# Kernel tuning notes

Measured on AMD Instinct MI355X. Metric: run time of the kernel, lower is better.

Reference implementation:

```python
import jax, jax.numpy as jnp
import numpy as np

D_MODEL = 1024
N_HEAD = 16
HEAD_DIM = D_MODEL // N_HEAD


def setup_inputs() -> dict:
    key = jax.random.key(0)
    ks = jax.random.split(key, 11)
    B, L = 1, 2048
    s = 1.0 / np.sqrt(D_MODEL)
    return {
        "q": jax.random.normal(ks[0], (B, L, D_MODEL), jnp.float32),
        "k": jax.random.normal(ks[1], (B, L, D_MODEL), jnp.float32),
        "v": jax.random.normal(ks[2], (B, L, D_MODEL), jnp.float32),
        "w_q": jax.random.normal(ks[3], (D_MODEL, D_MODEL), jnp.float32) * s,
        "b_q": jax.random.normal(ks[4], (D_MODEL,), jnp.float32) * s,
        "w_k": jax.random.normal(ks[5], (D_MODEL, D_MODEL), jnp.float32) * s,
        "b_k": jax.random.normal(ks[6], (D_MODEL,), jnp.float32) * s,
        "w_v": jax.random.normal(ks[7], (D_MODEL, D_MODEL), jnp.float32) * s,
        "b_v": jax.random.normal(ks[8], (D_MODEL,), jnp.float32) * s,
        "w_o": jax.random.normal(ks[9], (D_MODEL, D_MODEL), jnp.float32) * s,
        "b_o": jax.random.normal(ks[10], (D_MODEL,), jnp.float32) * s,
    }


def _split_heads(x):
    # [B, L, D] -> [B, H, L, Dh]
    B, L, D = x.shape
    return x.reshape(B, L, N_HEAD, HEAD_DIM).transpose(0, 2, 1, 3)


def reference(q, k, v, w_q, b_q, w_k, b_k, w_v, b_v, w_o, b_o):
    # Linear projections (torch Linear: x @ W.T + b; here weights stored as [D_in, D_out])
    qh = _split_heads(q @ w_q + b_q)
    kh = _split_heads(k @ w_k + b_k)
    vh = _split_heads(v @ w_v + b_v)
    scale = 1.0 / jnp.sqrt(jnp.asarray(HEAD_DIM, qh.dtype))
    # [B, H, Lq, Lk] full score matrix (faithful to naive implementation)
    score = jnp.einsum("bhqd,bhkd->bhqk", qh, kh) * scale
    attn = jax.nn.softmax(score, axis=-1)
    out = jnp.einsum("bhqk,bhkd->bhqd", attn, vh)
    # concat heads: [B, H, L, Dh] -> [B, L, D]
    B, H, L, Dh = out.shape
    out = out.transpose(0, 2, 1, 3).reshape(B, L, H * Dh)
    return out @ w_o + b_o  # dropout p=0.0 -> identity
```

## Files before the change

kernel.cpp:

```cpp
#include <hip/hip_runtime.h>
#include <hip/hip_bf16.h>
#include <stdint.h>
#include <stddef.h>

typedef __bf16 bf16_t;
typedef __bf16 v8bf __attribute__((ext_vector_type(8)));
typedef __bf16 v4bf __attribute__((ext_vector_type(4)));
typedef float  v4f  __attribute__((ext_vector_type(4)));

#define L_SEQ 2048
#define DM    1024
#define NH    16
#define LOG2E 1.44269504088896340736f
#define SCL   (0.125f * LOG2E)

__device__ __forceinline__ void async_cp16(const void* g, void* l) {
  __builtin_amdgcn_global_load_lds(
      (__attribute__((address_space(1))) void*)(g),
      (__attribute__((address_space(3))) void*)(l),
      16, 0, 0);
}

__device__ __forceinline__ v4f mfma16(v8bf a, v8bf b, v4f c) {
  return __builtin_amdgcn_mfma_f32_16x16x32_bf16(a, b, c, 0, 0, 0);
}

#if __has_builtin(__builtin_amdgcn_exp2f)
__device__ __forceinline__ float fast_exp2(float x) { return __builtin_amdgcn_exp2f(x); }
#else
__device__ __forceinline__ float fast_exp2(float x) { return exp2f(x); }
#endif

__global__ void k_prep(
    const float* __restrict__ q, const float* __restrict__ k,
    const float* __restrict__ v,
    const float* __restrict__ w0, const float* __restrict__ w1,
    const float* __restrict__ w2, const float* __restrict__ w3,
    bf16_t* __restrict__ Qb, bf16_t* __restrict__ Kb, bf16_t* __restrict__ Vb,
    bf16_t* __restrict__ o0, bf16_t* __restrict__ o1,
    bf16_t* __restrict__ o2, bf16_t* __restrict__ o3)
{
  const int z = blockIdx.z;
  const int tid = threadIdx.x;
  if (z < 4) {
    const float* in = (z == 0) ? w0 : (z == 1) ? w1 : (z == 2) ? w2 : w3;
    bf16_t*     out = (z == 0) ? o0 : (z == 1) ? o1 : (z == 2) ? o2 : o3;
    __shared__ float t[64 * 65];
    const int r0 = blockIdx.y * 64, c0 = blockIdx.x * 64;
#pragma unroll
    for (int p = 0; p < 16; ++p) {
      const int idx = p * 256 + tid;
      const int r = idx >> 6, c = idx & 63;
      t[r * 65 + c] = in[(size_t)(r0 + r) * DM + c0 + c];
    }
    __syncthreads();
#pragma unroll
    for (int p = 0; p < 16; ++p) {
      const int idx = p * 256 + tid;
      const int c = idx >> 6, r = idx & 63;
      out[(size_t)(c0 + c) * DM + r0 + r] = (bf16_t)t[r * 65 + c];
    }
  } else {
    const float* src = (z == 4) ? q : (z == 5) ? k : v;
    bf16_t*      dst = (z == 4) ? Qb : (z == 5) ? Kb : Vb;
    const int n4 = (L_SEQ * DM) / 4;
    const int base = (blockIdx.y * 16 + blockIdx.x) * 256 + tid;
#pragma unroll
    for (int i = base; i < n4; i += 16 * 16 * 256) {
      v4f x = ((const v4f*)src)[i];
      v4bf y;
      y[0] = (bf16_t)x[0]; y[1] = (bf16_t)x[1];
      y[2] = (bf16_t)x[2]; y[3] = (bf16_t)x[3];
      ((v4bf*)dst)[i] = y;
    }
  }
}

template <typename OutT>
__device__ __forceinline__ void gemm128x64_body(
    const bf16_t* __restrict__ A, const bf16_t* __restrict__ Bt,
    const float* __restrict__ biasN, const float* __restrict__ biasM,
    OutT* __restrict__ C, int M, int N, int K, int bx, int by)
{
  __shared__ __align__(16) bf16_t As[2][128 * 64];
  __shared__ __align__(16) bf16_t Bs[2][64 * 64];
  const int tid  = threadIdx.x;
  const int w    = tid >> 6;
  const int lane = tid & 63;
  const int l16  = lane & 15;
  const int q4   = lane >> 4;
  const int m0   = by * 128, n0 = bx * 64;
  const int wm   = (w >> 1) * 64, wn = (w & 1) * 32;
  const int lr = lane >> 3, lc = lane & 7;

  v4f acc[4][2];
#pragma unroll
  for (int i = 0; i < 4; ++i)
#pragma unroll
    for (int j = 0; j < 2; ++j) {
      v4f z = {0.f, 0.f, 0.f, 0.f};
      acc[i][j] = z;
    }

  auto stage = [&](int k0, int buf) {
#pragma unroll
    for (int c = 0; c < 4; ++c) {
      const int row = 32 * w + 8 * c + lr;
      const int q   = lc ^ (row & 7);
      async_cp16(A + (size_t)(m0 + row) * K + k0 + q * 8,
                 &As[buf][(32 * w + 8 * c) * 64]);
    }
#pragma unroll
    for (int c = 0; c < 2; ++c) {
      const int row = 16 * w + 8 * c + lr;
      const int q   = lc ^ (row & 7);
      async_cp16(Bt + (size_t)(n0 + row) * K + k0 + q * 8,
                 &Bs[buf][(16 * w + 8 * c) * 64]);
    }
  };

  stage(0, 0);
  __syncthreads();

  const int nk = K >> 6;
  for (int kt = 0; kt < nk; ++kt) {
    if (kt + 1 < nk) stage((kt + 1) << 6, (kt + 1) & 1);
    const int buf = kt & 1;
#pragma unroll
    for (int ks = 0; ks < 2; ++ks) {
      v8bf af[4], bf_[2];
#pragma unroll
      for (int mi = 0; mi < 4; ++mi) {
        const int row = wm + mi * 16 + l16;
        const int pc  = (4 * ks + q4) ^ (row & 7);
        af[mi] = *(const v8bf*)(&As[buf][row * 64 + pc * 8]);
      }
#pragma unroll
      for (int ni = 0; ni < 2; ++ni) {
        const int row = wn + ni * 16 + l16;
        const int pc  = (4 * ks + q4) ^ (row & 7);
        bf_[ni] = *(const v8bf*)(&Bs[buf][row * 64 + pc * 8]);
      }
#pragma unroll
      for (int mi = 0; mi < 4; ++mi)
#pragma unroll
        for (int ni = 0; ni < 2; ++ni)
          acc[mi][ni] = mfma16(af[mi], bf_[ni], acc[mi][ni]);
    }
    __syncthreads();
  }

  float bvn[2] = {0.f, 0.f};
  if (biasN) {
#pragma unroll
    for (int ni = 0; ni < 2; ++ni) bvn[ni] = biasN[n0 + wn + ni * 16 + l16];
  }
#pragma unroll
  for (int mi = 0; mi < 4; ++mi) {
#pragma unroll
    for (int r = 0; r < 4; ++r) {
      const int row = m0 + wm + mi * 16 + q4 * 4 + r;
      const float bm = biasM ? biasM[row] : 0.f;
#pragma unroll
      for (int ni = 0; ni < 2; ++ni) {
        const int col = n0 + wn + ni * 16 + l16;
        C[(size_t)row * N + col] = (OutT)(acc[mi][ni][r] + bvn[ni] + bm);
      }
    }
  }
}

__global__ __launch_bounds__(256, 3) void k_gemm_fused(
    const bf16_t* __restrict__ Qb, const bf16_t* __restrict__ Kb,
    const bf16_t* __restrict__ Vb,
    const bf16_t* __restrict__ Wqkt,
    const bf16_t* __restrict__ Wvt,
    const float* __restrict__ bq, const float* __restrict__ bk,
    const float* __restrict__ bv,
    bf16_t* __restrict__ QKo, bf16_t* __restrict__ Vtr)
{
  const int idx = blockIdx.x;
  const bf16_t *A, *Bt;
  const float *bN = nullptr, *bM = nullptr;
  bf16_t* C;
  int M, N, bx, by;
  if (idx < 512) {
    by = idx & 15; bx = idx >> 4;
    A  = (bx < 16) ? Qb : Kb;
    Bt = Wqkt;
    bN = (bx < 16) ? bq : (bk - DM);
    C  = QKo; M = L_SEQ; N = 2 * DM;
  } else {
    const int i2 = idx - 512;
    by = i2 & 7; bx = i2 >> 3;
    A  = Wvt; Bt = Vb; bM = bv;
    C  = Vtr; M = DM; N = L_SEQ;
  }
  gemm128x64_body<bf16_t>(A, Bt, bN, bM, C, M, N, DM, bx, by);
}

__global__ __launch_bounds__(256, 3) void k_gemm_oproj(
    const bf16_t* __restrict__ A, const bf16_t* __restrict__ Bt,
    const float* __restrict__ bias, float* __restrict__ C)
{
  gemm128x64_body<float>(A, Bt, bias, nullptr, C, L_SEQ, DM, DM,
                         blockIdx.x, blockIdx.y);
}

__global__ __launch_bounds__(128, 2) void k_attn(
    const bf16_t* __restrict__ QKp,
    const bf16_t* __restrict__ Vt,
    bf16_t* __restrict__ AO)
{
  constexpr int LD = 2 * DM;
  const int lid = blockIdx.x;
  const int h   = (lid & 7) + 8 * ((lid >> 3) & 1);
  const int q0  = (lid >> 4) * 32;
  const int tid = threadIdx.x, w = tid >> 6, lane = tid & 63;
  const int l16 = lane & 15, q4 = lane >> 4;
  const int lr = lane >> 3, lc = lane & 7;

  __shared__ __align__(16) bf16_t Ks[2][64 * 64];
  __shared__ __align__(16) bf16_t Vs[2][64 * 64];
  __shared__ __align__(16) bf16_t QPs[32 * 72];

  const bf16_t* Qp = QKp;
  const bf16_t* Kp = QKp + DM;

  const bf16_t* pK[4];
  const bf16_t* pV[4];
#pragma unroll
  for (int c = 0; c < 4; ++c) {
    const int row = 32 * w + 8 * c + lr;
    const int q   = lc ^ (row & 7);
    pK[c] = Kp + (size_t)row * LD + h * 64 + q * 8;
    pV[c] = Vt + (size_t)(h * 64 + row) * L_SEQ + q * 8;
  }
  auto stage_kv = [&](int j0, int buf) {
#pragma unroll
    for (int c = 0; c < 4; ++c) {
      async_cp16(pK[c] + (size_t)j0 * LD, &Ks[buf][(32 * w + 8 * c) * 64]);
      async_cp16(pV[c] + j0,              &Vs[buf][(32 * w + 8 * c) * 64]);
    }
  };

#pragma unroll
  for (int c = 0; c < 2; ++c) {
    const int row = 16 * w + 8 * c + lr;
    const int q   = lc ^ (row & 7);
    async_cp16(Qp + (size_t)(q0 + row) * LD + h * 64 + q * 8,
               &QPs[(16 * w + 8 * c) * 64]);
  }
  stage_kv(0, 0);
  __syncthreads();

  const int prow = 16 * w + l16;
  v8bf bq[2];
#pragma unroll
  for (int ks = 0; ks < 2; ++ks) {
    const int pc = (4 * ks + q4) ^ (prow & 7);
    bq[ks] = *(const v8bf*)(&QPs[prow * 64 + pc * 8]);
  }
  __syncthreads();

  float l_run = 0.f;
  v4f od[4];
#pragma unroll
  for (int d = 0; d < 4; ++d) { v4f z = {0.f, 0.f, 0.f, 0.f}; od[d] = z; }

  for (int jt = 0; jt < L_SEQ / 64; ++jt) {
    if (jt + 1 < L_SEQ / 64) stage_kv((jt + 1) * 64, (jt + 1) & 1);
    const int buf = jt & 1;

    v4f st[4];
#pragma unroll
    for (int nf = 0; nf < 4; ++nf) {
      v4f a0 = {0.f, 0.f, 0.f, 0.f};
      const int rowk = nf * 16 + l16;
#pragma unroll
      for (int ks = 0; ks < 2; ++ks) {
        const int pc = (4 * ks + q4) ^ (rowk & 7);
        v8bf ak = *(const v8bf*)(&Ks[buf][rowk * 64 + pc * 8]);
        a0 = mfma16(ak, bq[ks], a0);
      }
      st[nf] = a0;
    }

#pragma unroll
    for (int nf = 0; nf < 4; ++nf) {
      v4bf pb;
#pragma unroll
      for (int r = 0; r < 4; ++r) {
        const float p = fast_exp2(st[nf][r] * SCL);
        l_run += p;
        pb[r] = (bf16_t)p;
      }
      *(v4bf*)(&QPs[prow * 72 + nf * 16 + q4 * 4]) = pb;
    }

#pragma unroll
    for (int ks = 0; ks < 2; ++ks) {
      v8bf bp = *(const v8bf*)(&QPs[prow * 72 + ks * 32 + q4 * 8]);
#pragma unroll
      for (int dd = 0; dd < 4; ++dd) {
        const int rowv = dd * 16 + l16;
        const int pc   = (4 * ks + q4) ^ (rowv & 7);
        v8bf av = *(const v8bf*)(&Vs[buf][rowv * 64 + pc * 8]);
        od[dd] = mfma16(av, bp, od[dd]);
      }
    }
    __syncthreads();
  }

  l_run += __shfl_xor(l_run, 16, 64);
  l_run += __shfl_xor(l_run, 32, 64);
  const float inv = 1.f / l_run;
  const int rowo = q0 + prow;
#pragma unroll
  for (int dd = 0; dd < 4; ++dd) {
    v4bf ob;
#pragma unroll
    for (int r = 0; r < 4; ++r) ob[r] = (bf16_t)(od[dd][r] * inv);
    *(v4bf*)(&AO[(size_t)rowo * DM + h * 64 + dd * 16 + q4 * 4]) = ob;
  }
}

extern "C" void kernel_launch(void* const* d_in, const int* in_sizes, int n_in,
                              void* d_out, int out_size, void* d_ws, size_t ws_size,
                              hipStream_t stream)
{
  const float* q  = (const float*)d_in[0];
  const float* k  = (const float*)d_in[1];
  const float* v  = (const float*)d_in[2];
  const float* wq = (const float*)d_in[3];
  const float* bq = (const float*)d_in[4];
  const float* wk = (const float*)d_in[5];
  const float* bk = (const float*)d_in[6];
  const float* wv = (const float*)d_in[7];
  const float* bv = (const float*)d_in[8];
  const float* wo = (const float*)d_in[9];
  const float* bo = (const float*)d_in[10];
  float* out = (float*)d_out;

  const size_t SZ = (size_t)L_SEQ * DM;
  bf16_t* ws   = (bf16_t*)d_ws;
  bf16_t* Qb   = ws;
  bf16_t* Kb   = Qb + SZ;
  bf16_t* Vb   = Kb + SZ;
  bf16_t* QK   = Vb + SZ;
  bf16_t* Vtr  = QK + 2 * SZ;
  bf16_t* AO   = Vtr + SZ;
  bf16_t* Wqt  = AO + SZ;
  bf16_t* Wkt  = Wqt + (size_t)DM * DM;
  bf16_t* Wvt  = Wkt + (size_t)DM * DM;
  bf16_t* Wot  = Wvt + (size_t)DM * DM;

  k_prep<<<dim3(16, 16, 7), 256, 0, stream>>>(q, k, v, wq, wk, wv, wo,
                                              Qb, Kb, Vb, Wqt, Wkt, Wvt, Wot);
  k_gemm_fused<<<dim3(768), 256, 0, stream>>>(Qb, Kb, Vb, Wqt, Wvt,
                                              bq, bk, bv, QK, Vtr);
  k_attn<<<dim3(1024), 128, 0, stream>>>(QK, Vtr, AO);
  k_gemm_oproj<<<dim3(16, 16), 256, 0, stream>>>(AO, Wot, bo, out);
}
```

Before: 177.9 us.

## Split attention KV range across waves with 32x32 MFMA and cross-wave merge

Restructures the attention kernel so each of the two waves handles all 32 query rows against its own half of each 64-key tile, using 32x32x16 MFMA instead of 16x16x32. Each wave gets private double-buffered K/V staging and P scratch. Per-tile __syncthreads is replaced by explicit vmcnt waits, and the two waves' partial outputs and row sums are merged through LDS at the end. The aim is to cut LDS traffic and block-level barriers per tile, at the cost of larger accumulator register use and an extra reduction step.

```diff
diff --git a/kernel.cpp b/kernel.cpp
--- a/kernel.cpp
+++ b/kernel.cpp
@@ -7,6 +7,7 @@
 typedef __bf16 v8bf __attribute__((ext_vector_type(8)));
 typedef __bf16 v4bf __attribute__((ext_vector_type(4)));
 typedef float  v4f  __attribute__((ext_vector_type(4)));
+typedef float  v16f __attribute__((ext_vector_type(16)));
 
 #define L_SEQ 2048
 #define DM    1024
@@ -24,6 +25,16 @@
 __device__ __forceinline__ v4f mfma16(v8bf a, v8bf b, v4f c) {
   return __builtin_amdgcn_mfma_f32_16x16x32_bf16(a, b, c, 0, 0, 0);
 }
+__device__ __forceinline__ v16f mfma32(v8bf a, v8bf b, v16f c) {
+  return __builtin_amdgcn_mfma_f32_32x32x16_bf16(a, b, c, 0, 0, 0);
+}
+
+#define WAITVM(n)                                                          \
+  do {                                                                     \
+    __builtin_amdgcn_s_waitcnt((0xF << 8) | (0x7 << 4) | ((n) & 0xF) |     \
+                               ((((n) >> 4) & 3) << 14));                  \
+    __builtin_amdgcn_sched_barrier(0);                                     \
+  } while (0)
 
 #if __has_builtin(__builtin_amdgcn_exp2f)
 __device__ __forceinline__ float fast_exp2(float x) { return __builtin_amdgcn_exp2f(x); }
@@ -214,114 +225,129 @@
 {
   constexpr int LD = 2 * DM;
   const int lid = blockIdx.x;
-  const int h   = (lid & 7) + 8 * ((lid >> 3) & 1);
+  const int hd  = (lid & 7) + 8 * ((lid >> 3) & 1);
   const int q0  = (lid >> 4) * 32;
   const int tid = threadIdx.x, w = tid >> 6, lane = tid & 63;
-  const int l16 = lane & 15, q4 = lane >> 4;
-  const int lr = lane >> 3, lc = lane & 7;
-
-  __shared__ __align__(16) bf16_t Ks[2][64 * 64];
-  __shared__ __align__(16) bf16_t Vs[2][64 * 64];
-  __shared__ __align__(16) bf16_t QPs[32 * 72];
+  const int m31 = lane & 31;
+  const int hh  = lane >> 5;
+  const int lr8 = lane >> 3, lc8 = lane & 7;
+  const int lr4 = lane >> 2, lc4 = lane & 3;
+
+  __shared__ __align__(16) bf16_t KVs[2][2][2][32 * 64];
+  __shared__ __align__(16) bf16_t Ps2[2][32 * 34];
 
   const bf16_t* Qp = QKp;
   const bf16_t* Kp = QKp + DM;
 
-  const bf16_t* pK[4];
-  const bf16_t* pV[4];
-#pragma unroll
-  for (int c = 0; c < 4; ++c) {
-    const int row = 32 * w + 8 * c + lr;
-    const int q   = lc ^ (row & 7);
-    pK[c] = Kp + (size_t)row * LD + h * 64 + q * 8;
-    pV[c] = Vt + (size_t)(h * 64 + row) * L_SEQ + q * 8;
-  }
-  auto stage_kv = [&](int j0, int buf) {
+  const bf16_t* pK = Kp + (size_t)lr8 * LD + hd * 64 + (lc8 ^ lr8) * 8;
+  const bf16_t* pV = Vt + (size_t)(hd * 64 + lr4) * L_SEQ + (lc4 ^ (lr4 & 3)) * 8;
+
+  bf16_t* KbW = &KVs[w][0][0][0];
+  bf16_t* VbW = &KVs[w][1][0][0];
+
+  auto stage = [&](int i) {
+    const int j0  = 64 * i + 32 * w;
+    bf16_t* kb = KbW + (i & 1) * 2048;
+    bf16_t* vb = VbW + (i & 1) * 2048;
+#pragma unroll
+    for (int c = 0; c < 4; ++c)
+      async_cp16(pK + (size_t)(j0 + 8 * c) * LD, kb + (8 * c) * 64);
+#pragma unroll
+    for (int c = 0; c < 4; ++c)
+      async_cp16(pV + j0 + (size_t)(16 * c) * L_SEQ, vb + (16 * c) * 32);
+  };
+
+#pragma unroll
+  for (int c = 0; c < 2; ++c)
+    async_cp16(Qp + (size_t)(q0 + 16 * w + 8 * c + lr8) * LD + hd * 64 +
+                   (lc8 ^ lr8) * 8,
+               KbW + (8 * c) * 64);
+  __syncthreads();
+
+  v8bf bq[4];
+  {
+    const bf16_t* qrow = &KVs[m31 >> 4][0][0][(m31 & 15) * 64];
+#pragma unroll
+    for (int c = 0; c < 4; ++c)
+      bq[c] = *(const v8bf*)(qrow + (((2 * c + hh) ^ (m31 & 7)) * 8));
+  }
+  __syncthreads();
+
+  v16f od[2];
+#pragma unroll
+  for (int e = 0; e < 16; ++e) { od[0][e] = 0.f; od[1][e] = 0.f; }
+  float l_run = 0.f;
+
+  stage(0);
+
+  for (int i = 0; i < 32; ++i) {
+    if (i + 1 < 32) { stage(i + 1); WAITVM(8); } else { WAITVM(0); }
+    const bf16_t* kb = KbW + (i & 1) * 2048;
+    const bf16_t* vb = VbW + (i & 1) * 2048;
+
+    v16f st;
+#pragma unroll
+    for (int e = 0; e < 16; ++e) st[e] = 0.f;
 #pragma unroll
     for (int c = 0; c < 4; ++c) {
-      async_cp16(pK[c] + (size_t)j0 * LD, &Ks[buf][(32 * w + 8 * c) * 64]);
-      async_cp16(pV[c] + j0,              &Vs[buf][(32 * w + 8 * c) * 64]);
-    }
-  };
-
-#pragma unroll
-  for (int c = 0; c < 2; ++c) {
-    const int row = 16 * w + 8 * c + lr;
-    const int q   = lc ^ (row & 7);
-    async_cp16(Qp + (size_t)(q0 + row) * LD + h * 64 + q * 8,
-               &QPs[(16 * w + 8 * c) * 64]);
-  }
-  stage_kv(0, 0);
-  __syncthreads();
-
-  const int prow = 16 * w + l16;
-  v8bf bq[2];
-#pragma unroll
-  for (int ks = 0; ks < 2; ++ks) {
-    const int pc = (4 * ks + q4) ^ (prow & 7);
-    bq[ks] = *(const v8bf*)(&QPs[prow * 64 + pc * 8]);
-  }
-  __syncthreads();
-
-  float l_run = 0.f;
-  v4f od[4];
-#pragma unroll
-  for (int d = 0; d < 4; ++d) { v4f z = {0.f, 0.f, 0.f, 0.f}; od[d] = z; }
-
-  for (int jt = 0; jt < L_SEQ / 64; ++jt) {
-    if (jt + 1 < L_SEQ / 64) stage_kv((jt + 1) * 64, (jt + 1) & 1);
-    const int buf = jt & 1;
-
-    v4f st[4];
-#pragma unroll
-    for (int nf = 0; nf < 4; ++nf) {
-      v4f a0 = {0.f, 0.f, 0.f, 0.f};
-      const int rowk = nf * 16 + l16;
-#pragma unroll
-      for (int ks = 0; ks < 2; ++ks) {
-        const int pc = (4 * ks + q4) ^ (rowk & 7);
-        v8bf ak = *(const v8bf*)(&Ks[buf][rowk * 64 + pc * 8]);
-        a0 = mfma16(ak, bq[ks], a0);
-      }
-      st[nf] = a0;
-    }
-
-#pragma unroll
-    for (int nf = 0; nf < 4; ++nf) {
+      v8bf ak = *(const v8bf*)(kb + m31 * 64 + (((2 * c + hh) ^ (m31 & 7)) * 8));
+      st = mfma32(ak, bq[c], st);
+    }
+
+    bf16_t* prow = &Ps2[w][m31 * 34];
+#pragma unroll
+    for (int c = 0; c < 4; ++c) {
       v4bf pb;
 #pragma unroll
       for (int r = 0; r < 4; ++r) {
-        const float p = fast_exp2(st[nf][r] * SCL);
+        const float p = fast_exp2(st[4 * c + r] * SCL);
         l_run += p;
         pb[r] = (bf16_t)p;
       }
-      *(v4bf*)(&QPs[prow * 72 + nf * 16 + q4 * 4]) = pb;
-    }
-
-#pragma unroll
-    for (int ks = 0; ks < 2; ++ks) {
-      v8bf bp = *(const v8bf*)(&QPs[prow * 72 + ks * 32 + q4 * 8]);
-#pragma unroll
-      for (int dd = 0; dd < 4; ++dd) {
-        const int rowv = dd * 16 + l16;
-        const int pc   = (4 * ks + q4) ^ (rowv & 7);
-        v8bf av = *(const v8bf*)(&Vs[buf][rowv * 64 + pc * 8]);
-        od[dd] = mfma16(av, bp, od[dd]);
-      }
-    }
-    __syncthreads();
-  }
-
-  l_run += __shfl_xor(l_run, 16, 64);
+      *(v4bf*)(prow + 4 * hh + 8 * c) = pb;
+    }
+
+#pragma unroll
+    for (int c2 = 0; c2 < 2; ++c2) {
+      v8bf bp = *(const v8bf*)(prow + 16 * c2 + 8 * hh);
+#pragma unroll
+      for (int kk = 0; kk < 2; ++kk) {
+        const int d = 32 * (kk ^ w) + m31;
+        v8bf av = *(const v8bf*)(vb + d * 32 + (((2 * c2 + hh) ^ (d & 3)) * 8));
+        od[kk] = mfma32(av, bp, od[kk]);
+      }
+    }
+  }
+
   l_run += __shfl_xor(l_run, 32, 64);
-  const float inv = 1.f / l_run;
-  const int rowo = q0 + prow;
-#pragma unroll
-  for (int dd = 0; dd < 4; ++dd) {
+  __syncthreads();
+  float* ex  = (float*)&KVs[w][0][0][0];
+  float* lex = (float*)&Ps2[0][0];
+#pragma unroll
+  for (int c = 0; c < 4; ++c) {
+    v4f t;
+#pragma unroll
+    for (int r = 0; r < 4; ++r) t[r] = od[1][4 * c + r];
+    *(v4f*)(ex + c * 256 + lane * 4) = t;
+  }
+  lex[w * 64 + lane] = l_run;
+  __syncthreads();
+  const float* exp_ = (const float*)&KVs[1 - w][0][0][0];
+#pragma unroll
+  for (int c = 0; c < 4; ++c) {
+    v4f t = *(const v4f*)(exp_ + c * 256 + lane * 4);
+#pragma unroll
+    for (int r = 0; r < 4; ++r) od[0][4 * c + r] += t[r];
+  }
+  const float inv = 1.f / (l_run + lex[(1 - w) * 64 + lane]);
+
+  bf16_t* ao = AO + (size_t)(q0 + m31) * DM + hd * 64 + 32 * w + 4 * hh;
+#pragma unroll
+  for (int c = 0; c < 4; ++c) {
     v4bf ob;
 #pragma unroll
-    for (int r = 0; r < 4; ++r) ob[r] = (bf16_t)(od[dd][r] * inv);
-    *(v4bf*)(&AO[(size_t)rowo * DM + h * 64 + dd * 16 + q4 * 4]) = ob;
+    for (int r = 0; r < 4; ++r) ob[r] = (bf16_t)(od[0][4 * c + r] * inv);
+    *(v4bf*)(ao + 8 * c) = ob;
   }
 }
 
```

Result: slower. 213.5 us (+20.0%).
